# Kernel optimization log

Measured on AMD Instinct MI355X. Metric: run time of the kernel, lower is better.

Reference implementation:

```python
import jax, jax.numpy as jnp
import numpy as np

D_MODEL = 1024
N_HEADS = 16
D_K = 64  # per-head dim and the scaling denominator used by the module
NEG = -1e9  # stand-in for -inf in masked_fill (rows are never fully masked)


def setup_inputs() -> dict:
    key = jax.random.key(0)
    ks = jax.random.split(key, 8)
    B, M, N = 2, 2048, 2048
    q = jax.random.normal(ks[0], (B, M, D_MODEL), dtype=jnp.float32)
    k = jax.random.normal(ks[1], (B, N, D_MODEL), dtype=jnp.float32)
    v = jax.random.normal(ks[2], (B, N, D_MODEL), dtype=jnp.float32)
    mask = jax.random.randint(ks[3], (B, M, N), 0, 2).astype(jnp.bool_)
    # xavier_uniform for square [d,d] weights: limit = sqrt(6/(d+d))
    lim = float(np.sqrt(6.0 / (D_MODEL + D_MODEL)))
    Wq = jax.random.uniform(ks[4], (D_MODEL, D_MODEL), jnp.float32, -lim, lim)
    Wk = jax.random.uniform(ks[5], (D_MODEL, D_MODEL), jnp.float32, -lim, lim)
    Wv = jax.random.uniform(ks[6], (D_MODEL, D_MODEL), jnp.float32, -lim, lim)
    Wo = jax.random.uniform(ks[7], (D_MODEL, D_MODEL), jnp.float32, -lim, lim)
    return {"q": q, "k": k, "v": v, "mask": mask,
            "Wq": Wq, "Wk": Wk, "Wv": Wv, "Wo": Wo}


def _split_heads(x):
    # (B, S, D) -> (B, H, S, Dh); the torch split/cat-on-batch trick is
    # mathematically identical to this standard head reshape.
    B, S, _ = x.shape
    return x.reshape(B, S, N_HEADS, D_K).transpose(0, 2, 1, 3)


def reference(q, k, v, mask, Wq, Wk, Wv, Wo):
    qw = _split_heads(q @ Wq.T)  # (B,H,M,Dh)
    kw = _split_heads(k @ Wk.T)  # (B,H,N,Dh)
    vw = _split_heads(v @ Wv.T)  # (B,H,N,Dh)
    scores = jnp.einsum('bhmd,bhnd->bhmn', qw, kw)
    scores = jnp.where(mask[:, None, :, :], NEG, scores)
    attn = jax.nn.softmax(scores / jnp.sqrt(jnp.float32(D_K)), axis=-1)
    ctx = jnp.einsum('bhmn,bhnd->bhmd', attn, vw)
    B, _, M, _ = ctx.shape
    ctx = ctx.transpose(0, 2, 1, 3).reshape(B, M, D_MODEL)
    return ctx @ Wo.T
```

## Files before the change

kernel.cpp:

```cpp
#include <hip/hip_runtime.h>
#include <hip/hip_bf16.h>
#include <stdint.h>
#include <string.h>

#define SEQ   2048
#define DM    1024
#define NH    16
#define NB    2

typedef __attribute__((ext_vector_type(8))) short bf16x8;
typedef __attribute__((ext_vector_type(4))) float f32x4;
typedef unsigned short u16;
typedef unsigned int   u32;

__device__ __forceinline__ u16 f2bf(float f) {
    u32 u = __float_as_uint(f);
    u += 0x7FFF + ((u >> 16) & 1);
    return (u16)(u >> 16);
}
__device__ __forceinline__ u32 pk2bf(float a, float b) {
    __hip_bfloat162 p = __float22bfloat162_rn(make_float2(a, b));
    u32 u; memcpy(&u, &p, 4); return u;
}
__device__ __forceinline__ float fexp2(float x) {
#if __has_builtin(__builtin_amdgcn_exp2f)
    return __builtin_amdgcn_exp2f(x);
#else
    return exp2f(x);
#endif
}
__device__ __forceinline__ float mask_exp2(float s, u32 lsel, int pos) {
#if __has_builtin(__builtin_amdgcn_sbfe)
    u32 keep = (u32)__builtin_amdgcn_sbfe((int)lsel, pos, 1);
#else
    u32 keep = (u32)((int)(lsel << (31 - pos)) >> 31);
#endif
    return __uint_as_float(__float_as_uint(fexp2(s)) & keep);
}
__device__ __forceinline__ void gl_lds16(const void* g, void* l) {
    __builtin_amdgcn_global_load_lds(
        (const __attribute__((address_space(1))) u32*)g,
        (__attribute__((address_space(3))) u32*)l, 16, 0, 0);
}
__device__ __forceinline__ void wbar_vm3() { asm volatile("s_waitcnt vmcnt(3)\ns_barrier" ::: "memory"); }
__device__ __forceinline__ void wbar_vm4() { asm volatile("s_waitcnt vmcnt(4)\ns_barrier" ::: "memory"); }
__device__ __forceinline__ void vm_drain() { asm volatile("s_waitcnt vmcnt(0)" ::: "memory"); }

struct CvtArgs {
    const float* s[7];
    u16* d[7];
    float scale[7];
    int start[8];
};
__global__ __launch_bounds__(256) void cvt_kernel(CvtArgs a) {
    int bid = blockIdx.x;
    int seg = 0;
#pragma unroll
    for (int i = 1; i < 7; ++i) if (bid >= a.start[i]) seg = i;
    float sc = a.scale[seg];
    size_t base = (size_t)(bid - a.start[seg]) * 2048 + threadIdx.x * 8;
    const float4* s4 = (const float4*)(a.s[seg] + base);
    float4 x = s4[0], y = s4[1];
    u32 r[4];
    r[0] = pk2bf(x.x*sc, x.y*sc); r[1] = pk2bf(x.z*sc, x.w*sc);
    r[2] = pk2bf(y.x*sc, y.y*sc); r[3] = pk2bf(y.z*sc, y.w*sc);
    *(uint4*)(a.d[seg] + base) = *(uint4*)r;
}

__global__ void maskpack_kernel(const int* __restrict__ mask,
                                unsigned int* __restrict__ bits) {
    int gid = blockIdx.x * 256 + threadIdx.x;
    int m = mask[gid];
    unsigned long long bal = __ballot(m != 0);
    int lane = threadIdx.x & 63;
    if (lane == 0)       bits[gid >> 5] = (u32)(bal & 0xFFFFFFFFull);
    else if (lane == 32) bits[gid >> 5] = (u32)(bal >> 32);
}

template<int RT>
__device__ __forceinline__ void gemm_body(const u16* __restrict__ A,
                                          const u16* __restrict__ Bm,
                                          void* __restrict__ Y,
                                          int rtile, int ctile, int mode,
                                          u16* sA, u16* sB) {
    constexpr int ABUF = RT * 32 * 32;
    constexpr int BBUF = 128 * 32;
    const int tid  = threadIdx.x;
    const int wv   = tid >> 6, lane = tid & 63;
    const int quad = lane >> 4, ln = lane & 15;
    const int wr   = wv >> 1,  wc  = wv & 1;

    const int lr4 = lane >> 2;
    const int lcc = ((lane & 3) ^ ((lane >> 3) & 3)) * 8;

    const u16* gA[RT/2]; u16* lA[RT/2];
#pragma unroll
    for (int s = 0; s < RT/2; ++s) {
        int seg = wv * (RT/2) + s;
        gA[s] = A + (size_t)(rtile * (RT*32) + seg*16 + lr4) * 1024 + lcc;
        lA[s] = sA + seg * 512;
    }
    const u16* gB[2]; u16* lB[2];
#pragma unroll
    for (int s = 0; s < 2; ++s) {
        int seg = wv * 2 + s;
        gB[s] = Bm + (size_t)(ctile * 128 + seg*16 + lr4) * 1024 + lcc;
        lB[s] = sB + seg * 512;
    }

    f32x4 acc[RT][4];
#pragma unroll
    for (int i = 0; i < RT; ++i)
#pragma unroll
        for (int j = 0; j < 4; ++j) acc[i][j] = (f32x4){0.f,0.f,0.f,0.f};

    const int c0 = (quad ^ ((ln >> 1) & 3)) * 8;

#pragma unroll
    for (int s = 0; s < RT/2; ++s) gl_lds16(gA[s], lA[s]);
#pragma unroll
    for (int s = 0; s < 2; ++s)    gl_lds16(gB[s], lB[s]);
#pragma unroll
    for (int s = 0; s < RT/2; ++s) gl_lds16(gA[s] + 32, lA[s] + ABUF);
#pragma unroll
    for (int s = 0; s < 2; ++s)    gl_lds16(gB[s] + 32, lB[s] + BBUF);

    int bc = 0, bp = 2;
    for (int kt = 0; kt < 32; ++kt) {
        if (RT == 4) wbar_vm4(); else wbar_vm3();
        int pk = (kt + 2) & 31;
#pragma unroll
        for (int s = 0; s < RT/2; ++s) gl_lds16(gA[s] + pk*32, lA[s] + bp*ABUF);
#pragma unroll
        for (int s = 0; s < 2; ++s)    gl_lds16(gB[s] + pk*32, lB[s] + bp*BBUF);

        const u16* sAb = sA + bc * ABUF;
        const u16* sBb = sB + bc * BBUF;
        bf16x8 af[RT], bfr[4];
#pragma unroll
        for (int rt = 0; rt < RT; ++rt)
            af[rt] = *(const bf16x8*)(sAb + (wr*(RT*16) + rt*16 + ln) * 32 + c0);
#pragma unroll
        for (int ct = 0; ct < 4; ++ct)
            bfr[ct] = *(const bf16x8*)(sBb + (wc*64 + ct*16 + ln) * 32 + c0);
#pragma unroll
        for (int rt = 0; rt < RT; ++rt)
#pragma unroll
            for (int ct = 0; ct < 4; ++ct)
                acc[rt][ct] = __builtin_amdgcn_mfma_f32_16x16x32_bf16(
                    af[rt], bfr[ct], acc[rt][ct], 0, 0, 0);

        bc = (bc == 2) ? 0 : bc + 1;
        bp = (bp == 2) ? 0 : bp + 1;
    }
    vm_drain();

#pragma unroll
    for (int rt = 0; rt < RT; ++rt) {
#pragma unroll
        for (int ct = 0; ct < 4; ++ct) {
#pragma unroll
            for (int i = 0; i < 4; ++i) {
                int R = rtile*(RT*32) + wr*(RT*16) + rt*16 + quad*4 + i;
                int C = ctile*128 + wc*64 + ct*16 + ln;
                float val = acc[rt][ct][i];
                if (mode == 0) {
                    int b = R >> 11, s = R & 2047, h = C >> 6, d = C & 63;
                    ((u16*)Y)[((size_t)((b*NH + h) * SEQ + s) << 6) + d] = f2bf(val);
                } else if (mode == 1) {
                    int h = R >> 6, d = R & 63, b = C >> 11, n = C & 2047;
                    ((u16*)Y)[((size_t)((b*NH + h) * 64 + d) << 11) + n] = f2bf(val);
                } else {
                    ((float*)Y)[(size_t)R * 1024 + C] = val;
                }
            }
        }
    }
}

struct QKVArgs { const u16* A[3]; const u16* B[3]; u16* Y[3]; };

__global__ __launch_bounds__(256) void gemm_qkv(QKVArgs g) {
    __shared__ u16 sA[3 * 128 * 32];
    __shared__ u16 sB[3 * 128 * 32];
    int z = blockIdx.z;
    if (z == 2)
        gemm_body<4>(g.A[2], g.B[2], g.Y[2], blockIdx.y, blockIdx.x, 1, sA, sB);
    else
        gemm_body<4>(g.A[z], g.B[z], g.Y[z], blockIdx.x, blockIdx.y, 0, sA, sB);
}

__global__ __launch_bounds__(256) void gemm_out(const u16* __restrict__ A,
                                                const u16* __restrict__ Bm,
                                                float* __restrict__ Y) {
    __shared__ u16 sA[3 * 64 * 32];
    __shared__ u16 sB[3 * 128 * 32];
    gemm_body<2>(A, Bm, Y, blockIdx.x, blockIdx.y, 2, sA, sB);
}

__global__ __launch_bounds__(512, 6) void attn_kernel(
    const u16* __restrict__ qw,
    const u16* __restrict__ kw,
    const u16* __restrict__ vt,
    const u32* __restrict__ mbits,
    u16* __restrict__ ctx) {

    __shared__ u16 sK[3 * 4096];
    __shared__ u16 sV[3 * 4096];

    const int mtile = blockIdx.x;
    const int bh    = blockIdx.y;
    const int b     = bh >> 4;
    const int tid   = threadIdx.x;
    const int wv    = tid >> 6, lane = tid & 63;
    const int quad  = lane >> 4, ln = lane & 15;
    const int m0    = mtile * 128;

    const size_t hbase = (size_t)bh * SEQ * 64;

    bf16x8 qf[2];
    {
        const u16* qp = qw + hbase + (size_t)(m0 + wv*16 + ln) * 64 + quad*8;
        qf[0] = *(const bf16x8*)(qp);
        qf[1] = *(const bf16x8*)(qp + 32);
    }

    f32x4 o[4], lsum;
    lsum = (f32x4){0.f,0.f,0.f,0.f};
#pragma unroll
    for (int j = 0; j < 4; ++j) o[j] = (f32x4){0.f,0.f,0.f,0.f};

    bf16x8 ones;
#pragma unroll
    for (int i = 0; i < 8; ++i) ones[i] = (short)0x3F80;

    const u32* mrow = mbits + (size_t)(b*SEQ + m0 + wv*16 + ln) * 64;

    const int lr = lane >> 3;
    const int lc = (lane & 7) ^ lr;
    const u16* gK = kw + hbase + (size_t)(wv*8 + lr) * 64 + lc*8;
    const u16* gV = vt + hbase + (size_t)(wv*8 + lr) * SEQ + lc*8;
    u16* lK = sK + wv * 512;
    u16* lV = sV + wv * 512;

    const int c0 = (quad ^ (ln & 7)) * 8;

    const int qh = quad >> 1, h4 = (quad & 1) * 4, sw = ln & 7;
    const int cA0 = ((qh    ) ^ sw) * 8 + h4;
    const int cA1 = ((qh + 2) ^ sw) * 8 + h4;
    const int cB0 = ((qh + 4) ^ sw) * 8 + h4;
    const int cB1 = ((qh + 6) ^ sw) * 8 + h4;

    gl_lds16(gK, lK);
    gl_lds16(gV, lV);
    uint2 wwA = *(const uint2*)(mrow);
    gl_lds16(gK + 4096, lK + 4096);
    gl_lds16(gV + 64,   lV + 4096);
    uint2 wwB = *(const uint2*)(mrow + 2);

    int bc = 0, bp = 2;
    for (int nt = 0; nt < SEQ / 64; ++nt) {
        wbar_vm3();
        int pidx = (nt + 2) & 31;
        gl_lds16(gK + (size_t)pidx * 4096, lK + bp*4096);
        gl_lds16(gV + pidx * 64,           lV + bp*4096);
        uint2 wwC = *(const uint2*)(mrow + pidx*2);

        const u16* sKb = sK + bc * 4096;
        const u16* sVb = sV + bc * 4096;

        f32x4 s4[4];
#pragma unroll
        for (int ct = 0; ct < 4; ++ct) {
            const u16* kp = sKb + (ct*16 + ln) * 64;
            bf16x8 k0 = *(const bf16x8*)(kp + c0);
            bf16x8 k1 = *(const bf16x8*)(kp + (c0 ^ 32));
            f32x4 z = (f32x4){0.f, 0.f, 0.f, 0.f};
            z = __builtin_amdgcn_mfma_f32_16x16x32_bf16(k0, qf[0], z, 0, 0, 0);
            z = __builtin_amdgcn_mfma_f32_16x16x32_bf16(k1, qf[1], z, 0, 0, 0);
            s4[ct] = z;
        }

        u32 P0[4], P1[4];
        {
            u32 l0 = ~(wwA.x >> (quad * 4));
            u32 l1 = ~(wwA.y >> (quad * 4));
#pragma unroll
            for (int ct = 0; ct < 4; ++ct) {
                u32 lsel = (ct & 2) ? l1 : l0;
                float p[4];
#pragma unroll
                for (int i = 0; i < 4; ++i)
                    p[i] = mask_exp2(s4[ct][i], lsel, (ct & 1) * 16 + i);
                u32 lo = pk2bf(p[0], p[1]);
                u32 hi = pk2bf(p[2], p[3]);
                if (ct == 0)      { P0[0] = lo; P0[1] = hi; }
                else if (ct == 1) { P0[2] = lo; P0[3] = hi; }
                else if (ct == 2) { P1[0] = lo; P1[1] = hi; }
                else              { P1[2] = lo; P1[3] = hi; }
            }
        }
        bf16x8 pf0, pf1;
        memcpy(&pf0, P0, 16);
        memcpy(&pf1, P1, 16);

        lsum = __builtin_amdgcn_mfma_f32_16x16x32_bf16(pf0, ones, lsum, 0, 0, 0);
        lsum = __builtin_amdgcn_mfma_f32_16x16x32_bf16(pf1, ones, lsum, 0, 0, 0);
#pragma unroll
        for (int ct = 0; ct < 4; ++ct) {
            const u16* vrow = sVb + (ct*16 + ln) * 64;
            uint2 a0 = *(const uint2*)(vrow + cA0);
            uint2 a1 = *(const uint2*)(vrow + cA1);
            uint2 b0 = *(const uint2*)(vrow + cB0);
            uint2 b1 = *(const uint2*)(vrow + cB1);
            u32 V0[4] = {a0.x, a0.y, a1.x, a1.y};
            u32 V1[4] = {b0.x, b0.y, b1.x, b1.y};
            bf16x8 vf0, vf1;
            memcpy(&vf0, V0, 16);
            memcpy(&vf1, V1, 16);
            o[ct] = __builtin_amdgcn_mfma_f32_16x16x32_bf16(pf0, vf0, o[ct], 0, 0, 0);
            o[ct] = __builtin_amdgcn_mfma_f32_16x16x32_bf16(pf1, vf1, o[ct], 0, 0, 0);
        }

        wwA = wwB; wwB = wwC;
        bc = (bc == 2) ? 0 : bc + 1;
        bp = (bp == 2) ? 0 : bp + 1;
    }
    vm_drain();

#pragma unroll
    for (int i = 0; i < 4; ++i) {
        float inv = 1.f / lsum[i];
        int m = m0 + wv*16 + quad*4 + i;
        size_t base = ((size_t)(b * SEQ + m) << 10) + (bh & 15) * 64;
#pragma unroll
        for (int ct = 0; ct < 4; ++ct)
            ctx[base + ct*16 + ln] = f2bf(o[ct][i] * inv);
    }
}

extern "C" void kernel_launch(void* const* d_in, const int* in_sizes, int n_in,
                              void* d_out, int out_size, void* d_ws, size_t ws_size,
                              hipStream_t stream) {
    const float* q    = (const float*)d_in[0];
    const float* k    = (const float*)d_in[1];
    const float* v    = (const float*)d_in[2];
    const int*   mask = (const int*)d_in[3];
    const float* Wq   = (const float*)d_in[4];
    const float* Wk   = (const float*)d_in[5];
    const float* Wv   = (const float*)d_in[6];
    const float* Wo   = (const float*)d_in[7];
    float* out = (float*)d_out;

    char* ws = (char*)d_ws;
    const size_t SZH = (size_t)NB * SEQ * DM * 2;
    const size_t SZW = (size_t)DM * DM * 2;
    u16* qw   = (u16*)(ws);
    u16* kw   = (u16*)(ws + SZH);
    u16* vt   = (u16*)(ws + 2*SZH);
    u16* ctx  = (u16*)(ws + 3*SZH);
    u16* vb   = ctx;
    u32* mbits= (u32*)(ws + 4*SZH);
    u16* qb   = (u16*)(ws + 4*SZH + (1u<<20));
    u16* kb   = (u16*)(ws + 4*SZH + (1u<<20) + SZH);
    u16* Wqb  = (u16*)(ws + 4*SZH + (1u<<20) + 2*SZH);
    u16* Wkb  = (u16*)((char*)Wqb + SZW);
    u16* Wvb  = (u16*)((char*)Wqb + 2*SZW);
    u16* Wob  = (u16*)((char*)Wqb + 3*SZW);

    const float CSC = 0.18033688011112042f;

    CvtArgs ca;
    ca.s[0]=q;  ca.d[0]=qb;  ca.scale[0]=1.f;
    ca.s[1]=k;  ca.d[1]=kb;  ca.scale[1]=1.f;
    ca.s[2]=v;  ca.d[2]=vb;  ca.scale[2]=1.f;
    ca.s[3]=Wq; ca.d[3]=Wqb; ca.scale[3]=CSC;
    ca.s[4]=Wk; ca.d[4]=Wkb; ca.scale[4]=1.f;
    ca.s[5]=Wv; ca.d[5]=Wvb; ca.scale[5]=1.f;
    ca.s[6]=Wo; ca.d[6]=Wob; ca.scale[6]=1.f;
    int st[8] = {0, 2048, 4096, 6144, 6656, 7168, 7680, 8192};
    for (int i = 0; i < 8; ++i) ca.start[i] = st[i];
    cvt_kernel<<<dim3(8192), dim3(256), 0, stream>>>(ca);

    maskpack_kernel<<<dim3(NB*SEQ*SEQ/256), dim3(256), 0, stream>>>(mask, mbits);

    QKVArgs ga;
    ga.A[0]=qb;  ga.B[0]=Wqb; ga.Y[0]=qw;
    ga.A[1]=kb;  ga.B[1]=Wkb; ga.Y[1]=kw;
    ga.A[2]=Wvb; ga.B[2]=vb;  ga.Y[2]=vt;
    gemm_qkv<<<dim3(32, 8, 3), dim3(256), 0, stream>>>(ga);

    attn_kernel<<<dim3(SEQ/128, NB*NH), dim3(512), 0, stream>>>(qw, kw, vt, mbits, ctx);

    gemm_out<<<dim3(64, 8), dim3(256), 0, stream>>>(ctx, Wob, out);
}
```

Measured before the change: 266.4 us.

## Permute V^T columns at store to allow 16-byte LDS reads; unroll 4-buffer ring

The V projection epilogue now writes each 64-column block of V^T in a permuted order. The attention kernel can then load V fragments with the same two 16-byte LDS reads used for K, instead of four 8-byte reads that were reassembled in registers. The K/V LDS ring grows from three to four buffers and is indexed statically by a 4-way unrolled inner loop, which removes the runtime buffer rotation. MFMA sections are wrapped in s_setprio, and occupancy is lowered to 4 blocks per CU because of the larger shared-memory footprint.

```diff
diff --git a/kernel.cpp b/kernel.cpp
--- a/kernel.cpp
+++ b/kernel.cpp
@@ -169,6 +169,10 @@
                     ((u16*)Y)[((size_t)((b*NH + h) * SEQ + s) << 6) + d] = f2bf(val);
                 } else if (mode == 1) {
                     int h = R >> 6, d = R & 63, b = C >> 11, n = C & 2047;
+                    int nl = n & 63;
+                    int np = (nl & 32) | (((nl & 15) >> 2) << 3) | (nl & 3)
+                           | ((nl & 16) >> 2);
+                    n = (n & ~63) | np;
                     ((u16*)Y)[((size_t)((b*NH + h) * 64 + d) << 11) + n] = f2bf(val);
                 } else {
                     ((float*)Y)[(size_t)R * 1024 + C] = val;
@@ -198,15 +202,16 @@
     gemm_body<2>(A, Bm, Y, blockIdx.x, blockIdx.y, 2, sA, sB);
 }
 
-__global__ __launch_bounds__(512, 6) void attn_kernel(
+__global__ __launch_bounds__(512, 4) void attn_kernel(
     const u16* __restrict__ qw,
     const u16* __restrict__ kw,
     const u16* __restrict__ vt,
     const u32* __restrict__ mbits,
     u16* __restrict__ ctx) {
 
-    __shared__ u16 sK[3 * 4096];
-    __shared__ u16 sV[3 * 4096];
+    __shared__ __align__(16) u16 smem[32768];
+    u16* sK = smem;
+    u16* sV = smem + 16384;
 
     const int mtile = blockIdx.x;
     const int bh    = blockIdx.y;
@@ -244,12 +249,8 @@
     u16* lV = sV + wv * 512;
 
     const int c0 = (quad ^ (ln & 7)) * 8;
-
-    const int qh = quad >> 1, h4 = (quad & 1) * 4, sw = ln & 7;
-    const int cA0 = ((qh    ) ^ sw) * 8 + h4;
-    const int cA1 = ((qh + 2) ^ sw) * 8 + h4;
-    const int cB0 = ((qh + 4) ^ sw) * 8 + h4;
-    const int cB1 = ((qh + 6) ^ sw) * 8 + h4;
+    const u16* a1 = smem + ln*64 + c0;
+    const u16* a2 = smem + ln*64 + (c0 ^ 32);
 
     gl_lds16(gK, lK);
     gl_lds16(gV, lV);
@@ -258,73 +259,67 @@
     gl_lds16(gV + 64,   lV + 4096);
     uint2 wwB = *(const uint2*)(mrow + 2);
 
-    int bc = 0, bp = 2;
-    for (int nt = 0; nt < SEQ / 64; ++nt) {
-        wbar_vm3();
-        int pidx = (nt + 2) & 31;
-        gl_lds16(gK + (size_t)pidx * 4096, lK + bp*4096);
-        gl_lds16(gV + pidx * 64,           lV + bp*4096);
-        uint2 wwC = *(const uint2*)(mrow + pidx*2);
-
-        const u16* sKb = sK + bc * 4096;
-        const u16* sVb = sV + bc * 4096;
-
-        f32x4 s4[4];
-#pragma unroll
-        for (int ct = 0; ct < 4; ++ct) {
-            const u16* kp = sKb + (ct*16 + ln) * 64;
-            bf16x8 k0 = *(const bf16x8*)(kp + c0);
-            bf16x8 k1 = *(const bf16x8*)(kp + (c0 ^ 32));
-            f32x4 z = (f32x4){0.f, 0.f, 0.f, 0.f};
-            z = __builtin_amdgcn_mfma_f32_16x16x32_bf16(k0, qf[0], z, 0, 0, 0);
-            z = __builtin_amdgcn_mfma_f32_16x16x32_bf16(k1, qf[1], z, 0, 0, 0);
-            s4[ct] = z;
+    for (int mi = 0; mi < 8; ++mi) {
+#pragma unroll
+        for (int u = 0; u < 4; ++u) {
+            const int bc = u;
+            const int wb = (u + 2) & 3;
+            wbar_vm3();
+            int pidx = (mi*4 + u + 2) & 31;
+            gl_lds16(gK + (size_t)pidx * 4096, lK + wb*4096);
+            gl_lds16(gV + pidx * 64,           lV + wb*4096);
+            uint2 wwC = *(const uint2*)(mrow + pidx*2);
+
+            f32x4 s4[4];
+            __builtin_amdgcn_s_setprio(1);
+#pragma unroll
+            for (int ct = 0; ct < 4; ++ct) {
+                bf16x8 k0 = *(const bf16x8*)(a1 + bc*4096 + ct*1024);
+                bf16x8 k1 = *(const bf16x8*)(a2 + bc*4096 + ct*1024);
+                f32x4 z = (f32x4){0.f, 0.f, 0.f, 0.f};
+                z = __builtin_amdgcn_mfma_f32_16x16x32_bf16(k0, qf[0], z, 0, 0, 0);
+                z = __builtin_amdgcn_mfma_f32_16x16x32_bf16(k1, qf[1], z, 0, 0, 0);
+                s4[ct] = z;
+            }
+            __builtin_amdgcn_s_setprio(0);
+
+            u32 P0[4], P1[4];
+            {
+                u32 l0 = ~(wwA.x >> (quad * 4));
+                u32 l1 = ~(wwA.y >> (quad * 4));
+#pragma unroll
+                for (int ct = 0; ct < 4; ++ct) {
+                    u32 lsel = (ct & 2) ? l1 : l0;
+                    float p[4];
+#pragma unroll
+                    for (int i = 0; i < 4; ++i)
+                        p[i] = mask_exp2(s4[ct][i], lsel, (ct & 1) * 16 + i);
+                    u32 lo = pk2bf(p[0], p[1]);
+                    u32 hi = pk2bf(p[2], p[3]);
+                    if (ct == 0)      { P0[0] = lo; P0[1] = hi; }
+                    else if (ct == 1) { P0[2] = lo; P0[3] = hi; }
+                    else if (ct == 2) { P1[0] = lo; P1[1] = hi; }
+                    else              { P1[2] = lo; P1[3] = hi; }
+                }
+            }
+            bf16x8 pf0, pf1;
+            memcpy(&pf0, P0, 16);
+            memcpy(&pf1, P1, 16);
+
+            __builtin_amdgcn_s_setprio(1);
+            lsum = __builtin_amdgcn_mfma_f32_16x16x32_bf16(pf0, ones, lsum, 0, 0, 0);
+            lsum = __builtin_amdgcn_mfma_f32_16x16x32_bf16(pf1, ones, lsum, 0, 0, 0);
+#pragma unroll
+            for (int ct = 0; ct < 4; ++ct) {
+                bf16x8 vf0 = *(const bf16x8*)(a1 + 16384 + bc*4096 + ct*1024);
+                bf16x8 vf1 = *(const bf16x8*)(a2 + 16384 + bc*4096 + ct*1024);
+                o[ct] = __builtin_amdgcn_mfma_f32_16x16x32_bf16(pf0, vf0, o[ct], 0, 0, 0);
+                o[ct] = __builtin_amdgcn_mfma_f32_16x16x32_bf16(pf1, vf1, o[ct], 0, 0, 0);
+            }
+            __builtin_amdgcn_s_setprio(0);
+
+            wwA = wwB; wwB = wwC;
         }
-
-        u32 P0[4], P1[4];
-        {
-            u32 l0 = ~(wwA.x >> (quad * 4));
-            u32 l1 = ~(wwA.y >> (quad * 4));
-#pragma unroll
-            for (int ct = 0; ct < 4; ++ct) {
-                u32 lsel = (ct & 2) ? l1 : l0;
-                float p[4];
-#pragma unroll
-                for (int i = 0; i < 4; ++i)
-                    p[i] = mask_exp2(s4[ct][i], lsel, (ct & 1) * 16 + i);
-                u32 lo = pk2bf(p[0], p[1]);
-                u32 hi = pk2bf(p[2], p[3]);
-                if (ct == 0)      { P0[0] = lo; P0[1] = hi; }
-                else if (ct == 1) { P0[2] = lo; P0[3] = hi; }
-                else if (ct == 2) { P1[0] = lo; P1[1] = hi; }
-                else              { P1[2] = lo; P1[3] = hi; }
-            }
-        }
-        bf16x8 pf0, pf1;
-        memcpy(&pf0, P0, 16);
-        memcpy(&pf1, P1, 16);
-
-        lsum = __builtin_amdgcn_mfma_f32_16x16x32_bf16(pf0, ones, lsum, 0, 0, 0);
-        lsum = __builtin_amdgcn_mfma_f32_16x16x32_bf16(pf1, ones, lsum, 0, 0, 0);
-#pragma unroll
-        for (int ct = 0; ct < 4; ++ct) {
-            const u16* vrow = sVb + (ct*16 + ln) * 64;
-            uint2 a0 = *(const uint2*)(vrow + cA0);
-            uint2 a1 = *(const uint2*)(vrow + cA1);
-            uint2 b0 = *(const uint2*)(vrow + cB0);
-            uint2 b1 = *(const uint2*)(vrow + cB1);
-            u32 V0[4] = {a0.x, a0.y, a1.x, a1.y};
-            u32 V1[4] = {b0.x, b0.y, b1.x, b1.y};
-            bf16x8 vf0, vf1;
-            memcpy(&vf0, V0, 16);
-            memcpy(&vf1, V1, 16);
-            o[ct] = __builtin_amdgcn_mfma_f32_16x16x32_bf16(pf0, vf0, o[ct], 0, 0, 0);
-            o[ct] = __builtin_amdgcn_mfma_f32_16x16x32_bf16(pf1, vf1, o[ct], 0, 0, 0);
-        }
-
-        wwA = wwB; wwB = wwC;
-        bc = (bc == 2) ? 0 : bc + 1;
-        bp = (bp == 2) ? 0 : bp + 1;
     }
     vm_drain();
 
```

Result: faster. 257.9 us (-3.2%).
